# Optimization experiments

Measured on AMD Instinct MI355X. Metric: run time of the kernel, lower is better.

The kernel has to match this reference:

```python
import jax, jax.numpy as jnp
from jax import lax
import numpy as np

B, T, IN_DIM = 32, 2048, 36
HIDDEN, CODE_DIM, N_CODES, STRIDE, N_RES = 256, 128, 1024, 4, 4
BETA = 0.25
GN_GROUPS = 8


def conv1d(x, w, b, stride=1, padding=0):
    # x: (B,C,T), w: (O,I,k) torch layout
    y = lax.conv_general_dilated(x, w, (stride,), [(padding, padding)],
                                 dimension_numbers=('NCH', 'OIH', 'NCH'))
    return y + b[None, :, None]


def conv_transpose1d(x, w, b, stride, padding):
    # torch ConvTranspose1d weight layout (in, out, k); output_padding=0 (stride even)
    k = w.shape[-1]
    w_t = jnp.transpose(jnp.flip(w, -1), (1, 0, 2))  # (out, in, k)
    y = lax.conv_general_dilated(x, w_t, (1,), [(k - 1 - padding, k - 1 - padding)],
                                 lhs_dilation=(stride,), dimension_numbers=('NCH', 'OIH', 'NCH'))
    return y + b[None, :, None]


def group_norm(x, gamma, beta, eps=1e-5):
    Bx, C, Tx = x.shape
    xg = x.reshape(Bx, GN_GROUPS, C // GN_GROUPS, Tx)
    mu = xg.mean(axis=(2, 3), keepdims=True)
    var = xg.var(axis=(2, 3), keepdims=True)
    xn = ((xg - mu) * lax.rsqrt(var + eps)).reshape(Bx, C, Tx)
    return xn * gamma[None, :, None] + beta[None, :, None]


def res_block(x, g1, be1, w1, b1, g2, be2, w2, b2):
    h = conv1d(jax.nn.silu(group_norm(x, g1, be1)), w1, b1, padding=1)
    h = conv1d(jax.nn.silu(group_norm(h, g2, be2)), w2, b2, padding=1)
    return x + h


def vq(z_e, codebook):
    # z_e: (B, C, K); nearest-neighbor + straight-through estimator
    Bx, C, K = z_e.shape
    z = z_e.transpose(0, 2, 1).reshape(-1, C)  # (B*K, C)
    dist = (z * z).sum(1, keepdims=True) + (codebook * codebook).sum(1)[None, :] - 2.0 * (z @ codebook.T)
    codes = jnp.argmin(dist, axis=1)  # (B*K,)
    z_q = codebook[codes].reshape(Bx, K, C).transpose(0, 2, 1)  # (B, C, K)
    z_q_st = z_e + lax.stop_gradient(z_q - z_e)
    loss_vq = jnp.mean((z_q - lax.stop_gradient(z_e)) ** 2) + BETA * jnp.mean((lax.stop_gradient(z_q) - z_e) ** 2)
    counts = jnp.zeros((N_CODES,), z_e.dtype).at[codes].add(1.0)
    avg = counts / z.shape[0]
    perplexity = jnp.exp(-jnp.sum(avg * jnp.log(avg + 1e-10)))
    return z_q_st, codes.reshape(Bx, K), loss_vq, perplexity


def _gather_pos(a):  # slices (0:18),(18:21),(27:30) -> 24 dims
    return jnp.concatenate([a[..., 0:18], a[..., 18:21], a[..., 27:30]], axis=-1)


def _gather_dir(a):  # slices (21:27),(30:36) -> 12 dims
    return jnp.concatenate([a[..., 21:27], a[..., 30:36]], axis=-1)


def setup_inputs() -> dict:
    ks = iter(jax.random.split(jax.random.key(0), 64))

    def nrm(shape, scale=1.0):
        return scale * jax.random.normal(next(ks), shape, jnp.float32)

    def cw(o, i, k):
        return nrm((o, i, k), 1.0 / np.sqrt(i * k))

    def rcw(n, o, i, k):
        return nrm((n, o, i, k), 1.0 / np.sqrt(i * k))

    inp = {
        'x': nrm((B, T, IN_DIM)),
        'hand_valid_mask': jax.random.uniform(next(ks), (B, T, 2), jnp.float32),
        'enc_in_w': cw(HIDDEN, IN_DIM, 3), 'enc_in_b': nrm((HIDDEN,), 0.01),
        'enc_gn1_g': 1.0 + nrm((N_RES, HIDDEN), 0.01), 'enc_gn1_b': nrm((N_RES, HIDDEN), 0.01),
        'enc_c1_w': rcw(N_RES, HIDDEN, HIDDEN, 3), 'enc_c1_b': nrm((N_RES, HIDDEN), 0.01),
        'enc_gn2_g': 1.0 + nrm((N_RES, HIDDEN), 0.01), 'enc_gn2_b': nrm((N_RES, HIDDEN), 0.01),
        'enc_c2_w': rcw(N_RES, HIDDEN, HIDDEN, 3), 'enc_c2_b': nrm((N_RES, HIDDEN), 0.01),
        'down_w': cw(HIDDEN, HIDDEN, 2 * STRIDE), 'down_b': nrm((HIDDEN,), 0.01),
        'enc_out_w': cw(CODE_DIM, HIDDEN, 1), 'enc_out_b': nrm((CODE_DIM,), 0.01),
        'codebook': jax.random.uniform(next(ks), (N_CODES, CODE_DIM), jnp.float32, -1.0 / N_CODES, 1.0 / N_CODES),
        'dec_in_w': cw(HIDDEN, CODE_DIM, 1), 'dec_in_b': nrm((HIDDEN,), 0.01),
        'up_w': nrm((HIDDEN, HIDDEN, 2 * STRIDE), 1.0 / np.sqrt(HIDDEN * 2 * STRIDE)), 'up_b': nrm((HIDDEN,), 0.01),
        'dec_gn1_g': 1.0 + nrm((N_RES, HIDDEN), 0.01), 'dec_gn1_b': nrm((N_RES, HIDDEN), 0.01),
        'dec_c1_w': rcw(N_RES, HIDDEN, HIDDEN, 3), 'dec_c1_b': nrm((N_RES, HIDDEN), 0.01),
        'dec_gn2_g': 1.0 + nrm((N_RES, HIDDEN), 0.01), 'dec_gn2_b': nrm((N_RES, HIDDEN), 0.01),
        'dec_c2_w': rcw(N_RES, HIDDEN, HIDDEN, 3), 'dec_c2_b': nrm((N_RES, HIDDEN), 0.01),
        'dec_out_w': cw(IN_DIM, HIDDEN, 3), 'dec_out_b': nrm((IN_DIM,), 0.01),
    }
    return inp


def reference(x, hand_valid_mask, enc_in_w, enc_in_b, enc_gn1_g, enc_gn1_b, enc_c1_w, enc_c1_b,
              enc_gn2_g, enc_gn2_b, enc_c2_w, enc_c2_b, down_w, down_b, enc_out_w, enc_out_b,
              codebook, dec_in_w, dec_in_b, up_w, up_b, dec_gn1_g, dec_gn1_b, dec_c1_w, dec_c1_b,
              dec_gn2_g, dec_gn2_b, dec_c2_w, dec_c2_b, dec_out_w, dec_out_b):
    Bx, Tx, _ = x.shape
    # ---- encode ----
    h = conv1d(x.transpose(0, 2, 1), enc_in_w, enc_in_b, padding=1)
    for i in range(N_RES):
        h = res_block(h, enc_gn1_g[i], enc_gn1_b[i], enc_c1_w[i], enc_c1_b[i],
                      enc_gn2_g[i], enc_gn2_b[i], enc_c2_w[i], enc_c2_b[i])
    h = conv1d(h, down_w, down_b, stride=STRIDE, padding=STRIDE // 2)
    z_e = conv1d(h, enc_out_w, enc_out_b)  # (B, CODE_DIM, K); latent mask is all-ones (no input_length)
    # ---- quantize ----
    z_q, codes, loss_vq, perplexity = vq(z_e, codebook)
    # ---- decode ----
    h = conv1d(z_q, dec_in_w, dec_in_b)
    h = conv_transpose1d(h, up_w, up_b, STRIDE, STRIDE // 2)
    for i in range(N_RES):
        h = res_block(h, dec_gn1_g[i], dec_gn1_b[i], dec_c1_w[i], dec_c1_b[i],
                      dec_gn2_g[i], dec_gn2_b[i], dec_c2_w[i], dec_c2_b[i])
    x_hat = conv1d(h, dec_out_w, dec_out_b, padding=1)[..., :Tx].transpose(0, 2, 1)  # (B,T,36)
    # ---- smooth-L1 position loss (mask of ones (B,T,1): denom = B*T) ----
    d = _gather_pos(x_hat) - _gather_pos(x)
    ad = jnp.abs(d)
    l1 = jnp.where(ad < 1.0, 0.5 * d * d, ad - 0.5)
    loss_recon_pos = l1.sum() / (Bx * Tx)
    # ---- cosine direction loss with hand validity mask ----
    x_vec = _gather_dir(x).reshape(Bx, Tx, 4, 3)
    h_vec = _gather_dir(x_hat).reshape(Bx, Tx, 4, 3)
    mL = hand_valid_mask[..., 0]
    mR = hand_valid_mask[..., 1]
    m_vec = jnp.stack([mL, mL, mR, mR], axis=-1)  # (B,T,4)
    eps = 1e-8
    xn = x_vec / (jnp.linalg.norm(x_vec, axis=-1, keepdims=True) + eps)
    hn = h_vec / (jnp.linalg.norm(h_vec, axis=-1, keepdims=True) + eps)
    cos = (xn * hn).sum(-1)
    loss_recon_dir = ((1.0 - cos) * m_vec).sum() / jnp.maximum(m_vec.sum(), 1.0)
    return x_hat, codes, loss_vq, perplexity, loss_recon_pos, loss_recon_dir
```

## Files before the change

kernel.cpp:

```cpp
#include <hip/hip_runtime.h>
#include <cstddef>
#include <cstdint>


#define TID ((int)threadIdx.x)
#define NB 32

__device__ __forceinline__ float silu_f(float y) { return y / (1.f + expf(-y)); }

__global__ void perm_oik_iko(const float* __restrict__ src, float* __restrict__ dst,
                             int R, int O, int I, int K) {
  int n = R * O * I * K;
  for (int idx = blockIdx.x * blockDim.x + TID; idx < n; idx += gridDim.x * blockDim.x) {
    int o = idx % O;
    int k = (idx / O) % K;
    int i = (idx / (O * K)) % I;
    int r = idx / (O * K * I);
    dst[idx] = src[((r * O + o) * I + i) * K + k];
  }
}

__global__ void perm_decout(const float* __restrict__ src, float* __restrict__ dst) {
  int n = 256 * 36 * 4;
  for (int idx = blockIdx.x * blockDim.x + TID; idx < n; idx += gridDim.x * blockDim.x) {
    int k = idx & 3;
    int o = (idx >> 2) % 36;
    int i = idx / 144;
    dst[idx] = (k < 3) ? src[(o * 256 + i) * 3 + k] : 0.f;
  }
}

__global__ void zero_k(float* p, int n) {
  int i = blockIdx.x * blockDim.x + TID;
  if (i < n) p[i] = 0.f;
}

__global__ void csq_f32(const float* __restrict__ cb, float* __restrict__ csq) {
  int j = blockIdx.x * blockDim.x + TID;
  if (j < 1024) {
    float s = 0.f;
    for (int c = 0; c < 128; c++) { float v = cb[j * 128 + c]; s += v * v; }
    csq[j] = s;
  }
}

__global__ __launch_bounds__(256) void gn_part_f32(const float* __restrict__ in, float* __restrict__ part) {
  int bg = blockIdx.x >> 2, q = blockIdx.x & 3;
  const float4* src = (const float4*)(in + ((size_t)bg << 16) + ((size_t)q << 14));
  float s1 = 0.f, s2 = 0.f;
  for (int f = TID; f < 4096; f += 256) {
    float4 v = src[f];
    s1 += v.x + v.y + v.z + v.w;
    s2 += v.x * v.x + v.y * v.y + v.z * v.z + v.w * v.w;
  }
  __shared__ float r1[256], r2[256];
  r1[TID] = s1; r2[TID] = s2;
  __syncthreads();
  for (int st = 128; st > 0; st >>= 1) {
    if (TID < st) { r1[TID] += r1[TID + st]; r2[TID] += r2[TID + st]; }
    __syncthreads();
  }
  if (TID == 0) { part[blockIdx.x * 2] = r1[0]; part[blockIdx.x * 2 + 1] = r2[0]; }
}

__global__ __launch_bounds__(256) void conv_in_k(const float* __restrict__ x, const float* __restrict__ wT,
                                                 const float* __restrict__ bias, float* __restrict__ out) {
  int b = blockIdx.x >> 5;
  int t0 = (blockIdx.x & 31) << 6;
  int o0 = blockIdx.y << 6;
  int tx = TID & 15, oy = TID >> 4;
  __shared__ float ins[36][68];
  __shared__ float wsl[36 * 192];
  for (int idx = TID; idx < 36 * 66; idx += 256) {
    int i = idx % 36, c = idx / 36;
    int t = t0 - 1 + c;
    float v = 0.f;
    if (t >= 0 && t < 2048) v = x[((size_t)(b * 2048 + t)) * 36 + i];
    ins[i][c] = v;
  }
  for (int idx = TID; idx < 36 * 192; idx += 256) {
    int o = idx & 63;
    int kk = (idx >> 6) % 3;
    int i = idx / 192;
    wsl[idx] = wT[(i * 3 + kk) * 256 + o0 + o];
  }
  __syncthreads();
  float acc[4][4];
#pragma unroll
  for (int m = 0; m < 4; m++)
#pragma unroll
    for (int n = 0; n < 4; n++) acc[m][n] = 0.f;
  for (int i = 0; i < 36; i++) {
    float xv[6];
    float4 x4 = *(const float4*)&ins[i][tx << 2];
    xv[0] = x4.x; xv[1] = x4.y; xv[2] = x4.z; xv[3] = x4.w;
    xv[4] = ins[i][(tx << 2) + 4];
    xv[5] = ins[i][(tx << 2) + 5];
    const float* wrow = &wsl[i * 192];
    float wv[3][4];
    *(float4*)wv[0] = *(const float4*)&wrow[oy << 2];
    *(float4*)wv[1] = *(const float4*)&wrow[64 + (oy << 2)];
    *(float4*)wv[2] = *(const float4*)&wrow[128 + (oy << 2)];
#pragma unroll
    for (int m = 0; m < 4; m++)
#pragma unroll
      for (int n = 0; n < 4; n++)
        acc[m][n] += wv[0][m] * xv[n] + wv[1][m] * xv[n + 1] + wv[2][m] * xv[n + 2];
  }
  int obase = o0 + (oy << 2);
#pragma unroll
  for (int m = 0; m < 4; m++) {
    int o = obase + m;
    float bv = bias[o];
    size_t rowo = (((size_t)((b << 8) + o)) << 11) + t0 + (tx << 2);
#pragma unroll
    for (int n = 0; n < 4; n++) out[rowo + n] = acc[m][n] + bv;
  }
}

__global__ __launch_bounds__(256, 2) void conv3_gn_k(const float* __restrict__ in, const float* __restrict__ part,
                                                     const float* __restrict__ gamma, const float* __restrict__ beta,
                                                     const float* __restrict__ wT, const float* __restrict__ bias,
                                                     const float* __restrict__ src, float* __restrict__ out) {
  int b = blockIdx.x >> 3;
  int t0 = (blockIdx.x & 7) << 8;
  int o0 = blockIdx.y << 7;
  int tx = TID & 15, oy = TID >> 4;
  __shared__ float ins[16][264];
  __shared__ float wsl[3 * 16 * 128];
  float acc[2][4][16];
#pragma unroll
  for (int h = 0; h < 2; h++)
#pragma unroll
    for (int m = 0; m < 4; m++)
#pragma unroll
      for (int n = 0; n < 16; n++) acc[h][m][n] = 0.f;
  for (int ic0 = 0; ic0 < 256; ic0 += 16) {
    int g = ic0 >> 5;
    const float* pp = part + ((size_t)((b << 3) + g)) * 8;
    float s1 = pp[0] + pp[2] + pp[4] + pp[6];
    float s2 = pp[1] + pp[3] + pp[5] + pp[7];
    float mu = s1 * (1.f / 65536.f);
    float var = s2 * (1.f / 65536.f) - mu * mu;
    float rs = rsqrtf(var + 1e-5f);
    __syncthreads();
    {
      int ch = ic0 + oy;
      float a = rs * gamma[ch];
      float bb = beta[ch] - mu * a;
      const float* grow = in + (((size_t)((b << 8) + ch)) << 11);
#pragma unroll
      for (int q = 0; q < 17; q++) {
        int c = tx + (q << 4);
        if (c < 260) {
          int t = t0 - 1 + c;
          float v = 0.f;
          if (t >= 0 && t < 2048) {
            float h = grow[t];
            float y = h * a + bb;
            v = y / (1.f + expf(-y));
          }
          ins[oy][c] = v;
        }
      }
    }
    for (int idx4 = TID; idx4 < 1536; idx4 += 256) {
      int o4 = (idx4 & 31) << 2;
      int i = (idx4 >> 5) & 15;
      int kk = idx4 >> 9;
      *(float4*)&wsl[(((kk << 4) + i) << 7) + o4] =
          *(const float4*)&wT[((ic0 + i) * 3 + kk) * 256 + o0 + o4];
    }
    __syncthreads();
    for (int i = 0; i < 16; i++) {
      float xq[4][6];
#pragma unroll
      for (int q = 0; q < 4; q++) {
        *(float4*)&xq[q][0] = *(const float4*)&ins[i][(q << 6) + (tx << 2)];
        *(float2*)&xq[q][4] = *(const float2*)&ins[i][(q << 6) + (tx << 2) + 4];
      }
      float wv[3][4], wb[3][4];
#pragma unroll
      for (int kk = 0; kk < 3; kk++) {
        const float* wrow = &wsl[((kk << 4) + i) << 7];
        *(float4*)wv[kk] = *(const float4*)&wrow[oy << 2];
        *(float4*)wb[kk] = *(const float4*)&wrow[64 + (oy << 2)];
      }
#pragma unroll
      for (int m = 0; m < 4; m++)
#pragma unroll
        for (int q = 0; q < 4; q++)
#pragma unroll
          for (int n = 0; n < 4; n++) {
            acc[0][m][(q << 2) + n] += wv[0][m] * xq[q][n] + wv[1][m] * xq[q][n + 1] + wv[2][m] * xq[q][n + 2];
            acc[1][m][(q << 2) + n] += wb[0][m] * xq[q][n] + wb[1][m] * xq[q][n + 1] + wb[2][m] * xq[q][n + 2];
          }
    }
  }
#pragma unroll
  for (int h = 0; h < 2; h++)
#pragma unroll
    for (int m = 0; m < 4; m++) {
      int o = o0 + (h << 6) + (oy << 2) + m;
      float bv = bias[o];
      size_t rowbase = (((size_t)((b << 8) + o)) << 11) + t0 + (tx << 2);
#pragma unroll
      for (int q = 0; q < 4; q++) {
        size_t row = rowbase + (q << 6);
#pragma unroll
        for (int n = 0; n < 4; n++) {
          float v = acc[h][m][(q << 2) + n] + bv;
          if (src) v += src[row + n];
          out[row + n] = v;
        }
      }
    }
}

__global__ __launch_bounds__(256) void conv_down_k(const float* __restrict__ in, const float* __restrict__ wT,
                                                   const float* __restrict__ bias, float* __restrict__ out) {
  int b = blockIdx.x >> 3;
  int to0 = (blockIdx.x & 7) << 6;
  int o0 = blockIdx.y << 6;
  int tx = TID & 15, oy = TID >> 4;
  __shared__ float ins[16][264];
  __shared__ float wsl[16 * 512];
  float acc[4][4];
#pragma unroll
  for (int m = 0; m < 4; m++)
#pragma unroll
    for (int n = 0; n < 4; n++) acc[m][n] = 0.f;
  for (int ic0 = 0; ic0 < 256; ic0 += 16) {
    __syncthreads();
    for (int idx = TID; idx < 16 * 260; idx += 256) {
      int r = idx / 260, c = idx % 260;
      int s = (to0 << 2) - 2 + c;
      float v = 0.f;
      if (s >= 0 && s < 2048) v = in[(((size_t)((b << 8) + ic0 + r)) << 11) + s];
      ins[r][c] = v;
    }
    for (int idx = TID; idx < 16 * 512; idx += 256) {
      int o = idx & 63;
      int kk = (idx >> 6) & 7;
      int i = idx >> 9;
      wsl[idx] = wT[((ic0 + i) * 8 + kk) * 256 + o0 + o];
    }
    __syncthreads();
#pragma unroll 2
    for (int i = 0; i < 16; i++) {
      float xv[20];
#pragma unroll
      for (int q = 0; q < 5; q++) *(float4*)&xv[q * 4] = *(const float4*)&ins[i][(tx << 4) + (q << 2)];
      float wv[8][4];
#pragma unroll
      for (int kk = 0; kk < 8; kk++) *(float4*)wv[kk] = *(const float4*)&wsl[(i << 9) + (kk << 6) + (oy << 2)];
#pragma unroll
      for (int n = 0; n < 4; n++)
#pragma unroll
        for (int kk = 0; kk < 8; kk++) {
          float xval = xv[(n << 2) + kk];
#pragma unroll
          for (int m = 0; m < 4; m++) acc[m][n] += wv[kk][m] * xval;
        }
    }
  }
  int obase = o0 + (oy << 2);
#pragma unroll
  for (int m = 0; m < 4; m++) {
    int o = obase + m;
    float bv = bias[o];
    size_t rowo = (((size_t)((b << 8) + o)) << 9) + to0 + (tx << 2);
#pragma unroll
    for (int n = 0; n < 4; n++) out[rowo + n] = acc[m][n] + bv;
  }
}

__global__ __launch_bounds__(256) void conv1x1_k(const float* __restrict__ in, const float* __restrict__ wIO,
                                                 const float* __restrict__ bias, float* __restrict__ out,
                                                 int Kc, int O) {
  int b = blockIdx.x >> 3;
  int t0 = (blockIdx.x & 7) << 6;
  int o0 = blockIdx.y << 6;
  int tx = TID & 15, oy = TID >> 4;
  __shared__ float xs[32][64];
  __shared__ float wsd[32][64];
  float acc[4][4];
#pragma unroll
  for (int m = 0; m < 4; m++)
#pragma unroll
    for (int n = 0; n < 4; n++) acc[m][n] = 0.f;
  for (int ic0 = 0; ic0 < Kc; ic0 += 32) {
    __syncthreads();
    for (int idx = TID; idx < 2048; idx += 256) {
      int r = idx >> 6, c = idx & 63;
      xs[r][c] = in[((size_t)(b * Kc + ic0 + r) << 9) + t0 + c];
      wsd[r][c] = wIO[(ic0 + r) * O + o0 + c];
    }
    __syncthreads();
#pragma unroll 8
    for (int i = 0; i < 32; i++) {
      float4 xvv = *(const float4*)&xs[i][tx << 2];
      float4 wvv = *(const float4*)&wsd[i][oy << 2];
      float xv[4] = {xvv.x, xvv.y, xvv.z, xvv.w};
      float wv[4] = {wvv.x, wvv.y, wvv.z, wvv.w};
#pragma unroll
      for (int m = 0; m < 4; m++)
#pragma unroll
        for (int n = 0; n < 4; n++) acc[m][n] += wv[m] * xv[n];
    }
  }
#pragma unroll
  for (int m = 0; m < 4; m++) {
    int o = o0 + (oy << 2) + m;
    float bv = bias[o];
    size_t rowo = ((size_t)(b * O + o) << 9) + t0 + (tx << 2);
#pragma unroll
    for (int n = 0; n < 4; n++) out[rowo + n] = acc[m][n] + bv;
  }
}

__global__ __launch_bounds__(256) void vq_tiled(const float* __restrict__ zE,
                                                const float* __restrict__ cb,
                                                const float* __restrict__ csq,
                                                int* __restrict__ codes) {
  int b = blockIdx.x >> 3;
  int t0 = (blockIdx.x & 7) << 6;
  int cq = TID & 15, pq = TID >> 4;
  __shared__ float Zs[128][66];
  __shared__ float Cs[64][129];
  __shared__ float zsqs[64];
  __shared__ float bd[64][17];
  __shared__ int bix[64][17];
  for (int idx = TID; idx < 128 * 64; idx += 256) {
    int c = idx >> 6, p = idx & 63;
    Zs[c][p] = zE[((size_t)(b * 128 + c) << 9) + t0 + p];
  }
  __syncthreads();
  if (TID < 64) {
    float s = 0.f;
    for (int c = 0; c < 128; c++) { float v = Zs[c][TID]; s += v * v; }
    zsqs[TID] = s;
  }
  float best[4];
  int bidx[4];
#pragma unroll
  for (int n = 0; n < 4; n++) { best[n] = 3.4e38f; bidx[n] = 0; }
  const int j0 = cq << 2;
  for (int cg = 0; cg < 16; cg++) {
    __syncthreads();
    for (int idx = TID; idx < 64 * 128; idx += 256) {
      int j = idx >> 7, c = idx & 127;
      Cs[j][c] = cb[((cg << 6) + j) * 128 + c];
    }
    __syncthreads();
    float acc[4][4];
#pragma unroll
    for (int u = 0; u < 4; u++)
#pragma unroll
      for (int n = 0; n < 4; n++) acc[u][n] = 0.f;
    for (int c = 0; c < 128; c++) {
      float4 zv4 = *(const float4*)&Zs[c][pq << 2];
      float zv[4] = {zv4.x, zv4.y, zv4.z, zv4.w};
      float cv[4];
#pragma unroll
      for (int u = 0; u < 4; u++) cv[u] = Cs[j0 + u][c];
#pragma unroll
      for (int u = 0; u < 4; u++)
#pragma unroll
        for (int n = 0; n < 4; n++) acc[u][n] += zv[n] * cv[u];
    }
#pragma unroll
    for (int u = 0; u < 4; u++) {
      int code = (cg << 6) + j0 + u;
      float cs_ = csq[code];
#pragma unroll
      for (int n = 0; n < 4; n++) {
        float A = zsqs[(pq << 2) + n] + cs_;
        float B = 2.0f * acc[u][n];
        float d = A - B;
        if (d < best[n]) { best[n] = d; bidx[n] = code; }
      }
    }
  }
  __syncthreads();
#pragma unroll
  for (int n = 0; n < 4; n++) { bd[(pq << 2) + n][cq] = best[n]; bix[(pq << 2) + n][cq] = bidx[n]; }
  __syncthreads();
  if (TID < 64) {
    float bb = bd[TID][0];
    int bj = bix[TID][0];
    for (int q = 1; q < 16; q++) {
      float d = bd[TID][q];
      int j = bix[TID][q];
      if (d < bb || (d == bb && j < bj)) { bb = d; bj = j; }
    }
    codes[(b << 9) + t0 + TID] = bj;
  }
}

__global__ void count_k(const int* __restrict__ codes, float* __restrict__ counts) {
  int n = blockIdx.x * blockDim.x + TID;
  if (n < 16384) atomicAdd(&counts[codes[n]], 1.f);
}

__global__ __launch_bounds__(256) void gather_k(const float* __restrict__ cb, const int* __restrict__ codes,
                                                const float* __restrict__ zE, float* __restrict__ zQ,
                                                float* __restrict__ vqsum) {
  double part = 0.;
  const int total = 32 * 128 * 512;
  for (int idx = blockIdx.x * blockDim.x + TID; idx < total; idx += gridDim.x * blockDim.x) {
    int t = idx & 511;
    int c = (idx >> 9) & 127;
    int b = idx >> 16;
    int code = codes[(b << 9) + t];
    float q = cb[code * 128 + c];
    double d = (double)q - (double)zE[idx];
    zQ[idx] = q;
    part += d * d;
  }
  __shared__ double red[256];
  red[TID] = part;
  __syncthreads();
  for (int st = 128; st > 0; st >>= 1) {
    if (TID < st) red[TID] += red[TID + st];
    __syncthreads();
  }
  if (TID == 0) atomicAdd(vqsum, (float)red[0]);
}

__global__ __launch_bounds__(256) void conv_up_k(const float* __restrict__ in, const float* __restrict__ w,
                                                 const float* __restrict__ bias, float* __restrict__ out) {
  int b = blockIdx.x / 17;
  int s0 = (blockIdx.x % 17) << 5;
  int o0 = blockIdx.y << 6;
  int tx = TID & 15, oy = TID >> 4;
  __shared__ float ins[16][36];
  __shared__ float wsl[16 * 512];
  float acc[2][4][4];
#pragma unroll
  for (int j = 0; j < 2; j++)
#pragma unroll
    for (int m = 0; m < 4; m++)
#pragma unroll
      for (int r = 0; r < 4; r++) acc[j][m][r] = 0.f;
  for (int ic0 = 0; ic0 < 256; ic0 += 16) {
    __syncthreads();
    for (int idx = TID; idx < 16 * 34; idx += 256) {
      int r = idx / 34, c = idx % 34;
      int s = s0 - 1 + c;
      float v = 0.f;
      if (s >= 0 && s < 512) v = in[(((size_t)((b << 8) + ic0 + r)) << 9) + s];
      ins[r][c] = v;
    }
    for (int idx = TID; idx < 8192; idx += 256) {
      int rr = idx & 3;
      int o = (idx >> 2) & 63;
      int h = (idx >> 8) & 1;
      int i = idx >> 9;
      wsl[idx] = w[(((size_t)(ic0 + i)) << 11) + ((size_t)(o0 + o) << 3) + (h << 2) + rr];
    }
    __syncthreads();
#pragma unroll 2
    for (int i = 0; i < 16; i++) {
      float x0 = ins[i][2 * tx], x1 = ins[i][2 * tx + 1], x2 = ins[i][2 * tx + 2];
#pragma unroll
      for (int m = 0; m < 4; m++) {
        int om = (oy << 2) + m;
        float4 wa4 = *(const float4*)&wsl[(i << 9) + (om << 2)];
        float4 wb4 = *(const float4*)&wsl[(i << 9) + 256 + (om << 2)];
        float wa[4] = {wa4.x, wa4.y, wa4.z, wa4.w};
        float wb[4] = {wb4.x, wb4.y, wb4.z, wb4.w};
#pragma unroll
        for (int r = 0; r < 4; r++) {
          acc[0][m][r] += x1 * wa[r] + x0 * wb[r];
          acc[1][m][r] += x2 * wa[r] + x1 * wb[r];
        }
      }
    }
  }
#pragma unroll
  for (int j = 0; j < 2; j++) {
    int s1 = s0 + (tx << 1) + j;
#pragma unroll
    for (int m = 0; m < 4; m++) {
      int o = o0 + (oy << 2) + m;
      float bv = bias[o];
#pragma unroll
      for (int r = 0; r < 4; r++) {
        int t = (s1 << 2) + r - 2;
        if (t >= 0 && t < 2048) out[(((size_t)((b << 8) + o)) << 11) + t] = acc[j][m][r] + bv;
      }
    }
  }
}

__global__ __launch_bounds__(256) void conv_out_k(const float* __restrict__ in, const float* __restrict__ wP,
                                                  const float* __restrict__ bias, float* __restrict__ xhat) {
  int b = blockIdx.x >> 5;
  int t0 = (blockIdx.x & 31) << 6;
  int tx = TID & 63, oy = TID >> 6;
  __shared__ float ins[32][68];
  __shared__ float wsl[32 * 144];
  float acc[9];
#pragma unroll
  for (int m = 0; m < 9; m++) acc[m] = 0.f;
  for (int ic0 = 0; ic0 < 256; ic0 += 32) {
    __syncthreads();
    for (int idx = TID; idx < 32 * 66; idx += 256) {
      int r = idx / 66, c = idx % 66;
      int t = t0 - 1 + c;
      float v = 0.f;
      if (t >= 0 && t < 2048) v = in[(((size_t)((b << 8) + ic0 + r)) << 11) + t];
      ins[r][c] = v;
    }
    for (int idx = TID; idx < 32 * 144; idx += 256) {
      wsl[idx] = wP[ic0 * 144 + idx];
    }
    __syncthreads();
#pragma unroll 4
    for (int i = 0; i < 32; i++) {
      float x0 = ins[i][tx], x1 = ins[i][tx + 1], x2 = ins[i][tx + 2];
#pragma unroll
      for (int m = 0; m < 9; m++) {
        int o = oy * 9 + m;
        float4 wv = *(const float4*)&wsl[(i * 36 + o) << 2];
        acc[m] += wv.x * x0 + wv.y * x1 + wv.z * x2;
      }
    }
  }
  size_t orow = ((size_t)(b << 11) + t0 + tx) * 36;
#pragma unroll
  for (int m = 0; m < 9; m++) {
    int o = oy * 9 + m;
    xhat[orow + o] = acc[m] + bias[o];
  }
}

__global__ __launch_bounds__(256) void loss_k(const float* __restrict__ x, const float* __restrict__ xh,
                                              const float* __restrict__ mask, float* __restrict__ scal) {
  float pos = 0.f, dir = 0.f, ms = 0.f;
  for (int n = blockIdx.x * blockDim.x + TID; n < 65536; n += gridDim.x * blockDim.x) {
    const float* xp = x + (size_t)n * 36;
    const float* hp = xh + (size_t)n * 36;
    float a[36], h[36];
#pragma unroll
    for (int d4 = 0; d4 < 36; d4 += 4) {
      *(float4*)&a[d4] = *(const float4*)&xp[d4];
      *(float4*)&h[d4] = *(const float4*)&hp[d4];
    }
#pragma unroll
    for (int d = 0; d < 36; d++) {
      if (d < 21 || (d >= 27 && d < 30)) {
        float df = h[d] - a[d];
        float ad = fabsf(df);
        pos += (ad < 1.f) ? 0.5f * df * df : ad - 0.5f;
      }
    }
    float mL = mask[2 * (size_t)n], mR = mask[2 * (size_t)n + 1];
    const int vb[4] = {21, 24, 30, 33};
    float mv[4] = {mL, mL, mR, mR};
#pragma unroll
    for (int v = 0; v < 4; v++) {
      int o = vb[v];
      float ax = a[o], ay = a[o + 1], az = a[o + 2];
      float hx = h[o], hy = h[o + 1], hz = h[o + 2];
      float an = sqrtf(ax * ax + ay * ay + az * az) + 1e-8f;
      float hn = sqrtf(hx * hx + hy * hy + hz * hz) + 1e-8f;
      float cs = (ax * hx + ay * hy + az * hz) / (an * hn);
      dir += (1.f - cs) * mv[v];
    }
    ms += 2.f * (mL + mR);
  }
  __shared__ float rp[256], rd[256], rm[256];
  rp[TID] = pos; rd[TID] = dir; rm[TID] = ms;
  __syncthreads();
  for (int st = 128; st > 0; st >>= 1) {
    if (TID < st) { rp[TID] += rp[TID + st]; rd[TID] += rd[TID + st]; rm[TID] += rm[TID + st]; }
    __syncthreads();
  }
  if (TID == 0) {
    atomicAdd(&scal[1], rp[0]);
    atomicAdd(&scal[2], rd[0]);
    atomicAdd(&scal[3], rm[0]);
  }
}

__global__ __launch_bounds__(256) void finalize_k(const float* __restrict__ counts, const float* __restrict__ scal,
                                                  float* __restrict__ tail) {
  __shared__ float red[256];
  float s = 0.f;
  for (int j = TID; j < 1024; j += 256) {
    float avg = counts[j] * (1.f / 16384.f);
    s += avg * logf(avg + 1e-10f);
  }
  red[TID] = s;
  __syncthreads();
  for (int st = 128; st > 0; st >>= 1) {
    if (TID < st) red[TID] += red[TID + st];
    __syncthreads();
  }
  if (TID == 0) {
    tail[0] = 1.25f * scal[0] * (1.f / 2097152.f);
    tail[1] = expf(-red[0]);
    tail[2] = scal[1] * (1.f / 65536.f);
    tail[3] = scal[2] / fmaxf(scal[3], 1.f);
  }
}

__global__ void codesf_k(const int* __restrict__ codes, float* __restrict__ o) {
  int n = blockIdx.x * blockDim.x + TID;
  if (n < 16384) o[n] = (float)codes[n];
}

extern "C" void kernel_launch(void* const* d_in, const int* in_sizes, int n_in,
                              void* d_out, int out_size, void* d_ws, size_t ws_size,
                              hipStream_t stream) {
  const float* x = (const float*)d_in[0];
  const float* mask = (const float*)d_in[1];
  const float* enc_in_w = (const float*)d_in[2];
  const float* enc_in_b = (const float*)d_in[3];
  const float* enc_gn1_g = (const float*)d_in[4];
  const float* enc_gn1_b = (const float*)d_in[5];
  const float* enc_c1_w = (const float*)d_in[6];
  const float* enc_c1_b = (const float*)d_in[7];
  const float* enc_gn2_g = (const float*)d_in[8];
  const float* enc_gn2_b = (const float*)d_in[9];
  const float* enc_c2_w = (const float*)d_in[10];
  const float* enc_c2_b = (const float*)d_in[11];
  const float* down_w = (const float*)d_in[12];
  const float* down_b = (const float*)d_in[13];
  const float* enc_out_w = (const float*)d_in[14];
  const float* enc_out_b = (const float*)d_in[15];
  const float* codebook = (const float*)d_in[16];
  const float* dec_in_w = (const float*)d_in[17];
  const float* dec_in_b = (const float*)d_in[18];
  const float* up_w = (const float*)d_in[19];
  const float* up_b = (const float*)d_in[20];
  const float* dec_gn1_g = (const float*)d_in[21];
  const float* dec_gn1_b = (const float*)d_in[22];
  const float* dec_c1_w = (const float*)d_in[23];
  const float* dec_c1_b = (const float*)d_in[24];
  const float* dec_gn2_g = (const float*)d_in[25];
  const float* dec_gn2_b = (const float*)d_in[26];
  const float* dec_c2_w = (const float*)d_in[27];
  const float* dec_c2_b = (const float*)d_in[28];
  const float* dec_out_w = (const float*)d_in[29];
  const float* dec_out_b = (const float*)d_in[30];

  char* W = (char*)d_ws;
  float* zE = (float*)(W + 0);
  float* zQ = (float*)(W + 8388608);
  int* codes = (int*)(W + 16777216);
  float* counts = (float*)(W + 16842752);
  float* scal = (float*)(W + 16846848);
  float* csq = (float*)(W + 16846880);
  float* part_f = (float*)(W + 16850976);
  float* wf_enc_in = (float*)(W + 16859168);
  float* wf_enc_c1 = (float*)(W + 16969760);
  float* wf_enc_c2 = (float*)(W + 20115488);
  float* wf_down = (float*)(W + 23261216);
  float* wf_enc_out = (float*)(W + 25358368);
  float* wf_dec_in = (float*)(W + 25489440);
  float* wf_dec_c1 = (float*)(W + 25620512);
  float* wf_dec_c2 = (float*)(W + 28766240);
  float* wf_dec_out = (float*)(W + 31911968);
  float* f0 = (float*)(W + 50331648);
  float* f2 = (float*)(W + 50331648 + (size_t)67108864);
  float* dech = (float*)(W + 50331648 + 2 * (size_t)67108864);

  dim3 blk(256);
  zero_k<<<dim3(5), blk, 0, stream>>>(counts, 1032);
  perm_oik_iko<<<dim3(128), blk, 0, stream>>>(enc_in_w, wf_enc_in, 1, 256, 36, 3);
  perm_oik_iko<<<dim3(1024), blk, 0, stream>>>(enc_c1_w, wf_enc_c1, 4, 256, 256, 3);
  perm_oik_iko<<<dim3(1024), blk, 0, stream>>>(enc_c2_w, wf_enc_c2, 4, 256, 256, 3);
  perm_oik_iko<<<dim3(1024), blk, 0, stream>>>(down_w, wf_down, 1, 256, 256, 8);
  perm_oik_iko<<<dim3(128), blk, 0, stream>>>(enc_out_w, wf_enc_out, 1, 128, 256, 1);
  perm_oik_iko<<<dim3(128), blk, 0, stream>>>(dec_in_w, wf_dec_in, 1, 256, 128, 1);
  perm_oik_iko<<<dim3(1024), blk, 0, stream>>>(dec_c1_w, wf_dec_c1, 4, 256, 256, 3);
  perm_oik_iko<<<dim3(1024), blk, 0, stream>>>(dec_c2_w, wf_dec_c2, 4, 256, 256, 3);
  perm_decout<<<dim3(64), blk, 0, stream>>>(dec_out_w, wf_dec_out);
  csq_f32<<<dim3(4), blk, 0, stream>>>(codebook, csq);

  const int GN = NB * 8 * 4;

  conv_in_k<<<dim3(NB * 32, 4), blk, 0, stream>>>(x, wf_enc_in, enc_in_b, f0);
  for (int i = 0; i < 4; i++) {
    gn_part_f32<<<dim3(GN), blk, 0, stream>>>(f0, part_f);
    conv3_gn_k<<<dim3(NB * 8, 2), blk, 0, stream>>>(f0, part_f, enc_gn1_g + i * 256, enc_gn1_b + i * 256,
                                                    wf_enc_c1 + i * 196608, enc_c1_b + i * 256, nullptr, f2);
    gn_part_f32<<<dim3(GN), blk, 0, stream>>>(f2, part_f);
    conv3_gn_k<<<dim3(NB * 8, 2), blk, 0, stream>>>(f2, part_f, enc_gn2_g + i * 256, enc_gn2_b + i * 256,
                                                    wf_enc_c2 + i * 196608, enc_c2_b + i * 256, f0, f0);
  }
  conv_down_k<<<dim3(NB * 8, 4), blk, 0, stream>>>(f0, wf_down, down_b, f2);
  conv1x1_k<<<dim3(NB * 8, 2), blk, 0, stream>>>(f2, wf_enc_out, enc_out_b, zE, 256, 128);

  vq_tiled<<<dim3(256), blk, 0, stream>>>(zE, codebook, csq, codes);
  count_k<<<dim3(64), blk, 0, stream>>>(codes, counts);
  gather_k<<<dim3(512), blk, 0, stream>>>(codebook, codes, zE, zQ, &scal[0]);

  float* xhat = (float*)d_out;
  conv1x1_k<<<dim3(NB * 8, 4), blk, 0, stream>>>(zQ, wf_dec_in, dec_in_b, dech, 128, 256);
  conv_up_k<<<dim3(NB * 17, 4), blk, 0, stream>>>(dech, up_w, up_b, f0);
  for (int i = 0; i < 4; i++) {
    gn_part_f32<<<dim3(GN), blk, 0, stream>>>(f0, part_f);
    conv3_gn_k<<<dim3(NB * 8, 2), blk, 0, stream>>>(f0, part_f, dec_gn1_g + i * 256, dec_gn1_b + i * 256,
                                                    wf_dec_c1 + i * 196608, dec_c1_b + i * 256, nullptr, f2);
    gn_part_f32<<<dim3(GN), blk, 0, stream>>>(f2, part_f);
    conv3_gn_k<<<dim3(NB * 8, 2), blk, 0, stream>>>(f2, part_f, dec_gn2_g + i * 256, dec_gn2_b + i * 256,
                                                    wf_dec_c2 + i * 196608, dec_c2_b + i * 256, f0, f0);
  }
  conv_out_k<<<dim3(NB * 32), blk, 0, stream>>>(f0, wf_dec_out, dec_out_b, xhat);

  loss_k<<<dim3(256), blk, 0, stream>>>(x, xhat, mask, scal);
  finalize_k<<<dim3(1), blk, 0, stream>>>(counts, scal, (float*)d_out + 2375680);
  codesf_k<<<dim3(64), blk, 0, stream>>>(codes, (float*)d_out + 2359296);
}
```

Before: 8.060 ms.

## Fuse GroupNorm statistics into conv epilogues and prefetch next input-channel tile

Removes the separate gn_part_f32 reduction passes by having each conv kernel (conv_in, conv3, conv_up) accumulate per-group sum and sum-of-squares of its output in the epilogue and atomically add them into a per-layer stats buffer. This avoids a full re-read of each 64MB activation tensor before every normalized conv. Separately, conv3_gn_k now register-prefetches the next 16-channel slice of inputs and weights while computing the current one, to hide global load latency. This costs extra registers in a kernel with launch bounds (256,2), plus atomics and a single-pass variance in float32 that is order-nondeterministic.

```diff
diff --git a/kernel.cpp b/kernel.cpp
--- a/kernel.cpp
+++ b/kernel.cpp
@@ -44,27 +44,9 @@
   }
 }
 
-__global__ __launch_bounds__(256) void gn_part_f32(const float* __restrict__ in, float* __restrict__ part) {
-  int bg = blockIdx.x >> 2, q = blockIdx.x & 3;
-  const float4* src = (const float4*)(in + ((size_t)bg << 16) + ((size_t)q << 14));
-  float s1 = 0.f, s2 = 0.f;
-  for (int f = TID; f < 4096; f += 256) {
-    float4 v = src[f];
-    s1 += v.x + v.y + v.z + v.w;
-    s2 += v.x * v.x + v.y * v.y + v.z * v.z + v.w * v.w;
-  }
-  __shared__ float r1[256], r2[256];
-  r1[TID] = s1; r2[TID] = s2;
-  __syncthreads();
-  for (int st = 128; st > 0; st >>= 1) {
-    if (TID < st) { r1[TID] += r1[TID + st]; r2[TID] += r2[TID + st]; }
-    __syncthreads();
-  }
-  if (TID == 0) { part[blockIdx.x * 2] = r1[0]; part[blockIdx.x * 2 + 1] = r2[0]; }
-}
-
 __global__ __launch_bounds__(256) void conv_in_k(const float* __restrict__ x, const float* __restrict__ wT,
-                                                 const float* __restrict__ bias, float* __restrict__ out) {
+                                                 const float* __restrict__ bias, float* __restrict__ out,
+                                                 float* __restrict__ partOut) {
   int b = blockIdx.x >> 5;
   int t0 = (blockIdx.x & 31) << 6;
   int o0 = blockIdx.y << 6;
@@ -108,20 +90,39 @@
         acc[m][n] += wv[0][m] * xv[n] + wv[1][m] * xv[n + 1] + wv[2][m] * xv[n + 2];
   }
   int obase = o0 + (oy << 2);
+  float s1 = 0.f, s2 = 0.f;
 #pragma unroll
   for (int m = 0; m < 4; m++) {
     int o = obase + m;
     float bv = bias[o];
     size_t rowo = (((size_t)((b << 8) + o)) << 11) + t0 + (tx << 2);
 #pragma unroll
-    for (int n = 0; n < 4; n++) out[rowo + n] = acc[m][n] + bv;
-  }
-}
-
-__global__ __launch_bounds__(256, 2) void conv3_gn_k(const float* __restrict__ in, const float* __restrict__ part,
+    for (int n = 0; n < 4; n++) {
+      float v = acc[m][n] + bv;
+      out[rowo + n] = v;
+      s1 += v; s2 += v * v;
+    }
+  }
+  __syncthreads();
+  float* red = (float*)ins;
+  red[TID] = s1; red[256 + TID] = s2;
+  __syncthreads();
+  for (int st = 64; st > 0; st >>= 1) {
+    if ((TID & 127) < st) { red[TID] += red[TID + st]; red[256 + TID] += red[256 + TID + st]; }
+    __syncthreads();
+  }
+  if ((TID & 127) == 0) {
+    int g = (blockIdx.y << 1) + (TID >> 7);
+    atomicAdd(&partOut[(((b << 3) + g) << 1)], red[TID]);
+    atomicAdd(&partOut[(((b << 3) + g) << 1) + 1], red[256 + TID]);
+  }
+}
+
+__global__ __launch_bounds__(256, 2) void conv3_gn_k(const float* __restrict__ in, const float* __restrict__ partIn,
                                                      const float* __restrict__ gamma, const float* __restrict__ beta,
                                                      const float* __restrict__ wT, const float* __restrict__ bias,
-                                                     const float* __restrict__ src, float* __restrict__ out) {
+                                                     const float* __restrict__ src, float* __restrict__ out,
+                                                     float* __restrict__ partOut) {
   int b = blockIdx.x >> 3;
   int t0 = (blockIdx.x & 7) << 8;
   int o0 = blockIdx.y << 7;
@@ -135,43 +136,86 @@
     for (int m = 0; m < 4; m++)
 #pragma unroll
       for (int n = 0; n < 16; n++) acc[h][m][n] = 0.f;
+
+  float xpre[17];
+  float4 wpre[6];
+  {
+    const float* grow = in + (((size_t)((b << 8) + oy)) << 11);
+#pragma unroll
+    for (int q = 0; q < 17; q++) {
+      int c = tx + (q << 4);
+      float v = 0.f;
+      if (c < 260) {
+        int t = t0 - 1 + c;
+        if (t >= 0 && t < 2048) v = grow[t];
+      }
+      xpre[q] = v;
+    }
+#pragma unroll
+    for (int j = 0; j < 6; j++) {
+      int idx4 = TID + (j << 8);
+      int o4 = (idx4 & 31) << 2;
+      int i = (idx4 >> 5) & 15;
+      int kk = idx4 >> 9;
+      wpre[j] = *(const float4*)&wT[(i * 3 + kk) * 256 + o0 + o4];
+    }
+  }
+
   for (int ic0 = 0; ic0 < 256; ic0 += 16) {
     int g = ic0 >> 5;
-    const float* pp = part + ((size_t)((b << 3) + g)) * 8;
-    float s1 = pp[0] + pp[2] + pp[4] + pp[6];
-    float s2 = pp[1] + pp[3] + pp[5] + pp[7];
+    const float* pp = partIn + (((size_t)((b << 3) + g)) << 1);
+    float s1 = pp[0], s2 = pp[1];
     float mu = s1 * (1.f / 65536.f);
     float var = s2 * (1.f / 65536.f) - mu * mu;
     float rs = rsqrtf(var + 1e-5f);
-    __syncthreads();
-    {
-      int ch = ic0 + oy;
-      float a = rs * gamma[ch];
-      float bb = beta[ch] - mu * a;
-      const float* grow = in + (((size_t)((b << 8) + ch)) << 11);
-#pragma unroll
-      for (int q = 0; q < 17; q++) {
-        int c = tx + (q << 4);
-        if (c < 260) {
-          int t = t0 - 1 + c;
-          float v = 0.f;
-          if (t >= 0 && t < 2048) {
-            float h = grow[t];
-            float y = h * a + bb;
-            v = y / (1.f + expf(-y));
-          }
-          ins[oy][c] = v;
+    int ch = ic0 + oy;
+    float a = rs * gamma[ch];
+    float bb = beta[ch] - mu * a;
+    __syncthreads();
+#pragma unroll
+    for (int q = 0; q < 17; q++) {
+      int c = tx + (q << 4);
+      if (c < 260) {
+        int t = t0 - 1 + c;
+        float v = 0.f;
+        if (t >= 0 && t < 2048) {
+          float y = xpre[q] * a + bb;
+          v = y / (1.f + expf(-y));
         }
-      }
-    }
-    for (int idx4 = TID; idx4 < 1536; idx4 += 256) {
+        ins[oy][c] = v;
+      }
+    }
+#pragma unroll
+    for (int j = 0; j < 6; j++) {
+      int idx4 = TID + (j << 8);
       int o4 = (idx4 & 31) << 2;
       int i = (idx4 >> 5) & 15;
       int kk = idx4 >> 9;
-      *(float4*)&wsl[(((kk << 4) + i) << 7) + o4] =
-          *(const float4*)&wT[((ic0 + i) * 3 + kk) * 256 + o0 + o4];
-    }
-    __syncthreads();
+      *(float4*)&wsl[(((kk << 4) + i) << 7) + o4] = wpre[j];
+    }
+    __syncthreads();
+    if (ic0 < 240) {
+      int icn = ic0 + 16;
+      const float* grow = in + (((size_t)((b << 8) + icn + oy)) << 11);
+#pragma unroll
+      for (int q = 0; q < 17; q++) {
+        int c = tx + (q << 4);
+        float v = 0.f;
+        if (c < 260) {
+          int t = t0 - 1 + c;
+          if (t >= 0 && t < 2048) v = grow[t];
+        }
+        xpre[q] = v;
+      }
+#pragma unroll
+      for (int j = 0; j < 6; j++) {
+        int idx4 = TID + (j << 8);
+        int o4 = (idx4 & 31) << 2;
+        int i = (idx4 >> 5) & 15;
+        int kk = idx4 >> 9;
+        wpre[j] = *(const float4*)&wT[((icn + i) * 3 + kk) * 256 + o0 + o4];
+      }
+    }
     for (int i = 0; i < 16; i++) {
       float xq[4][6];
 #pragma unroll
@@ -197,6 +241,7 @@
           }
     }
   }
+  float sh1[2] = {0.f, 0.f}, sh2[2] = {0.f, 0.f};
 #pragma unroll
   for (int h = 0; h < 2; h++)
 #pragma unroll
@@ -212,9 +257,27 @@
           float v = acc[h][m][(q << 2) + n] + bv;
           if (src) v += src[row + n];
           out[row + n] = v;
+          sh1[h] += v; sh2[h] += v * v;
         }
       }
     }
+  __syncthreads();
+  float* red = (float*)ins;
+#pragma unroll
+  for (int h = 0; h < 2; h++) {
+    red[TID] = sh1[h]; red[256 + TID] = sh2[h];
+    __syncthreads();
+    for (int st = 64; st > 0; st >>= 1) {
+      if ((TID & 127) < st) { red[TID] += red[TID + st]; red[256 + TID] += red[256 + TID + st]; }
+      __syncthreads();
+    }
+    if ((TID & 127) == 0) {
+      int g = (blockIdx.y << 2) + (h << 1) + (TID >> 7);
+      atomicAdd(&partOut[(((b << 3) + g) << 1)], red[TID]);
+      atomicAdd(&partOut[(((b << 3) + g) << 1) + 1], red[256 + TID]);
+    }
+    __syncthreads();
+  }
 }
 
 __global__ __launch_bounds__(256) void conv_down_k(const float* __restrict__ in, const float* __restrict__ wT,
@@ -429,7 +492,8 @@
 }
 
 __global__ __launch_bounds__(256) void conv_up_k(const float* __restrict__ in, const float* __restrict__ w,
-                                                 const float* __restrict__ bias, float* __restrict__ out) {
+                                                 const float* __restrict__ bias, float* __restrict__ out,
+                                                 float* __restrict__ partOut) {
   int b = blockIdx.x / 17;
   int s0 = (blockIdx.x % 17) << 5;
   int o0 = blockIdx.y << 6;
@@ -478,19 +542,37 @@
       }
     }
   }
+  float s1 = 0.f, s2 = 0.f;
 #pragma unroll
   for (int j = 0; j < 2; j++) {
-    int s1 = s0 + (tx << 1) + j;
+    int sS = s0 + (tx << 1) + j;
 #pragma unroll
     for (int m = 0; m < 4; m++) {
       int o = o0 + (oy << 2) + m;
       float bv = bias[o];
 #pragma unroll
       for (int r = 0; r < 4; r++) {
-        int t = (s1 << 2) + r - 2;
-        if (t >= 0 && t < 2048) out[(((size_t)((b << 8) + o)) << 11) + t] = acc[j][m][r] + bv;
-      }
-    }
+        int t = (sS << 2) + r - 2;
+        if (t >= 0 && t < 2048) {
+          float v = acc[j][m][r] + bv;
+          out[(((size_t)((b << 8) + o)) << 11) + t] = v;
+          s1 += v; s2 += v * v;
+        }
+      }
+    }
+  }
+  __syncthreads();
+  float* red = (float*)ins;
+  red[TID] = s1; red[256 + TID] = s2;
+  __syncthreads();
+  for (int st = 64; st > 0; st >>= 1) {
+    if ((TID & 127) < st) { red[TID] += red[TID + st]; red[256 + TID] += red[256 + TID + st]; }
+    __syncthreads();
+  }
+  if ((TID & 127) == 0) {
+    int g = (blockIdx.y << 1) + (TID >> 7);
+    atomicAdd(&partOut[(((b << 3) + g) << 1)], red[TID]);
+    atomicAdd(&partOut[(((b << 3) + g) << 1) + 1], red[256 + TID]);
   }
 }
 
@@ -653,23 +735,23 @@
   int* codes = (int*)(W + 16777216);
   float* counts = (float*)(W + 16842752);
   float* scal = (float*)(W + 16846848);
-  float* csq = (float*)(W + 16846880);
-  float* part_f = (float*)(W + 16850976);
-  float* wf_enc_in = (float*)(W + 16859168);
-  float* wf_enc_c1 = (float*)(W + 16969760);
-  float* wf_enc_c2 = (float*)(W + 20115488);
-  float* wf_down = (float*)(W + 23261216);
-  float* wf_enc_out = (float*)(W + 25358368);
-  float* wf_dec_in = (float*)(W + 25489440);
-  float* wf_dec_c1 = (float*)(W + 25620512);
-  float* wf_dec_c2 = (float*)(W + 28766240);
-  float* wf_dec_out = (float*)(W + 31911968);
+  float* stats = (float*)(W + 16846880);
+  float* csq = (float*)(W + 16883744);
+  float* wf_enc_in = (float*)(W + 16887840);
+  float* wf_enc_c1 = (float*)(W + 16998432);
+  float* wf_enc_c2 = (float*)(W + 20144160);
+  float* wf_down = (float*)(W + 23289888);
+  float* wf_enc_out = (float*)(W + 25387040);
+  float* wf_dec_in = (float*)(W + 25518112);
+  float* wf_dec_c1 = (float*)(W + 25649184);
+  float* wf_dec_c2 = (float*)(W + 28794912);
+  float* wf_dec_out = (float*)(W + 31940640);
   float* f0 = (float*)(W + 50331648);
   float* f2 = (float*)(W + 50331648 + (size_t)67108864);
   float* dech = (float*)(W + 50331648 + 2 * (size_t)67108864);
 
   dim3 blk(256);
-  zero_k<<<dim3(5), blk, 0, stream>>>(counts, 1032);
+  zero_k<<<dim3(41), blk, 0, stream>>>(counts, 1024 + 8 + 9216);
   perm_oik_iko<<<dim3(128), blk, 0, stream>>>(enc_in_w, wf_enc_in, 1, 256, 36, 3);
   perm_oik_iko<<<dim3(1024), blk, 0, stream>>>(enc_c1_w, wf_enc_c1, 4, 256, 256, 3);
   perm_oik_iko<<<dim3(1024), blk, 0, stream>>>(enc_c2_w, wf_enc_c2, 4, 256, 256, 3);
@@ -681,16 +763,15 @@
   perm_decout<<<dim3(64), blk, 0, stream>>>(dec_out_w, wf_dec_out);
   csq_f32<<<dim3(4), blk, 0, stream>>>(codebook, csq);
 
-  const int GN = NB * 8 * 4;
-
-  conv_in_k<<<dim3(NB * 32, 4), blk, 0, stream>>>(x, wf_enc_in, enc_in_b, f0);
+  conv_in_k<<<dim3(NB * 32, 4), blk, 0, stream>>>(x, wf_enc_in, enc_in_b, f0, stats + 0 * 512);
   for (int i = 0; i < 4; i++) {
-    gn_part_f32<<<dim3(GN), blk, 0, stream>>>(f0, part_f);
-    conv3_gn_k<<<dim3(NB * 8, 2), blk, 0, stream>>>(f0, part_f, enc_gn1_g + i * 256, enc_gn1_b + i * 256,
-                                                    wf_enc_c1 + i * 196608, enc_c1_b + i * 256, nullptr, f2);
-    gn_part_f32<<<dim3(GN), blk, 0, stream>>>(f2, part_f);
-    conv3_gn_k<<<dim3(NB * 8, 2), blk, 0, stream>>>(f2, part_f, enc_gn2_g + i * 256, enc_gn2_b + i * 256,
-                                                    wf_enc_c2 + i * 196608, enc_c2_b + i * 256, f0, f0);
+    float* sIn = stats + (2 * i) * 512;
+    float* sMid = stats + (2 * i + 1) * 512;
+    float* sOut = stats + (2 * i + 2) * 512;
+    conv3_gn_k<<<dim3(NB * 8, 2), blk, 0, stream>>>(f0, sIn, enc_gn1_g + i * 256, enc_gn1_b + i * 256,
+                                                    wf_enc_c1 + i * 196608, enc_c1_b + i * 256, nullptr, f2, sMid);
+    conv3_gn_k<<<dim3(NB * 8, 2), blk, 0, stream>>>(f2, sMid, enc_gn2_g + i * 256, enc_gn2_b + i * 256,
+                                                    wf_enc_c2 + i * 196608, enc_c2_b + i * 256, f0, f0, sOut);
   }
   conv_down_k<<<dim3(NB * 8, 4), blk, 0, stream>>>(f0, wf_down, down_b, f2);
   conv1x1_k<<<dim3(NB * 8, 2), blk, 0, stream>>>(f2, wf_enc_out, enc_out_b, zE, 256, 128);
@@ -701,14 +782,15 @@
 
   float* xhat = (float*)d_out;
   conv1x1_k<<<dim3(NB * 8, 4), blk, 0, stream>>>(zQ, wf_dec_in, dec_in_b, dech, 128, 256);
-  conv_up_k<<<dim3(NB * 17, 4), blk, 0, stream>>>(dech, up_w, up_b, f0);
+  conv_up_k<<<dim3(NB * 17, 4), blk, 0, stream>>>(dech, up_w, up_b, f0, stats + 9 * 512);
   for (int i = 0; i < 4; i++) {
-    gn_part_f32<<<dim3(GN), blk, 0, stream>>>(f0, part_f);
-    conv3_gn_k<<<dim3(NB * 8, 2), blk, 0, stream>>>(f0, part_f, dec_gn1_g + i * 256, dec_gn1_b + i * 256,
-                                                    wf_dec_c1 + i * 196608, dec_c1_b + i * 256, nullptr, f2);
-    gn_part_f32<<<dim3(GN), blk, 0, stream>>>(f2, part_f);
-    conv3_gn_k<<<dim3(NB * 8, 2), blk, 0, stream>>>(f2, part_f, dec_gn2_g + i * 256, dec_gn2_b + i * 256,
-                                                    wf_dec_c2 + i * 196608, dec_c2_b + i * 256, f0, f0);
+    float* sIn = stats + (9 + 2 * i) * 512;
+    float* sMid = stats + (10 + 2 * i) * 512;
+    float* sOut = stats + (11 + 2 * i) * 512;
+    conv3_gn_k<<<dim3(NB * 8, 2), blk, 0, stream>>>(f0, sIn, dec_gn1_g + i * 256, dec_gn1_b + i * 256,
+                                                    wf_dec_c1 + i * 196608, dec_c1_b + i * 256, nullptr, f2, sMid);
+    conv3_gn_k<<<dim3(NB * 8, 2), blk, 0, stream>>>(f2, sMid, dec_gn2_g + i * 256, dec_gn2_b + i * 256,
+                                                    wf_dec_c2 + i * 196608, dec_c2_b + i * 256, f0, f0, sOut);
   }
   conv_out_k<<<dim3(NB * 32), blk, 0, stream>>>(f0, wf_dec_out, dec_out_b, xhat);
 
```

New measurement: 7.988 ms. Within noise of the previous version (-0.9%).
